# Optimization experiments

Hardware: AMD Instinct MI355X
Metric: run time of the kernel (lower is better)

The kernel has to match this reference:

```python
import jax, jax.numpy as jnp
import numpy as np
from jax import lax

W_MAX = 8
STEP = 1
LEAK = 2
KSIZE = (W_MAX - 1) * (STEP + LEAK)  # 21 = kernel size, padding, and fodep
THETA = 80
FODEP = KSIZE
OUT_CH = 1
NEURONS = 1024


def make_w_kernel_table():
    # StepFireLeak response table: [w_max, ksize], flipped in time
    w_idx = np.arange(W_MAX, dtype=np.float32)[:, None]
    t_idx = np.arange(KSIZE, dtype=np.float32)[None, :]
    w_step = np.maximum(np.floor(1.0 + t_idx / STEP), 0.0)
    w_leak = np.maximum(np.ceil(w_idx + ((w_idx - 1.0) * STEP - t_idx) / LEAK), 0.0)
    table = np.minimum(w_step, w_leak).astype(np.int32)[:, ::-1]
    return jnp.asarray(np.ascontiguousarray(table))


def setup_inputs() -> dict:
    key = jax.random.key(0)
    k1, k2 = jax.random.split(key)
    B, C, S, T = 64, 1, 784, 500
    input_spikes = (jax.random.uniform(k1, (B, C, S, T)) < 0.05).astype(jnp.float32)
    # integer synaptic weights in [0, w_max)
    weight = jax.random.randint(k2, (OUT_CH * NEURONS, C * S), 0, W_MAX, dtype=jnp.int32)
    return {"input_spikes": input_spikes, "weight": weight}


def reference(input_spikes, weight):
    B, C, S, T = input_spikes.shape
    x = input_spikes.reshape(B, C * S, T)
    # expand integer weights into response kernels: [out, in, ksize]
    table = make_w_kernel_table().astype(jnp.float32)
    kern = table[weight]
    pot = lax.conv_general_dilated(
        x, kern, window_strides=(1,), padding=[(KSIZE, KSIZE)],
        dimension_numbers=("NCH", "OIH", "NCH"))
    pot = jnp.rint(pot).astype(jnp.int32)
    Tp = pot.shape[-1]  # T + ksize + 1
    pot = pot.reshape(B, OUT_CH, NEURONS, Tp)
    pot_t = jnp.transpose(pot, (3, 0, 1, 2))  # [Tp, B, C, N]

    def step(dep, p):  # dep: [B, C] int32, p: [B, C, N]
        winner = jnp.argmax(p, axis=-1)  # [B, C]
        val = jnp.take_along_axis(p, winner[..., None], axis=-1)[..., 0]
        cond = ((val > THETA) & (dep == 0)).astype(jnp.int32)  # min_depression == 0
        winners_t = jax.nn.one_hot(winner, NEURONS, dtype=jnp.int32) * cond[..., None]
        new_dep = jnp.maximum(0, dep + cond * (FODEP + 1) - 1)
        return new_dep, winners_t

    dep0 = jnp.zeros((B, OUT_CH), dtype=jnp.int32)
    _, winners = lax.scan(step, dep0, pot_t)  # [Tp, B, C, N]
    return jnp.transpose(winners, (1, 2, 3, 0))  # [B, C, N, Tp]
```

## Files before the change

kernel.cpp:

```cpp
#include <hip/hip_runtime.h>

#define B_DIM 64
#define S_DIM 784
#define T_DIM 500
#define N_DIM 1024
#define TP    522
#define KS    21
#define THETA 80
#define NCHUNK 8
#define CH    66
#define LISTCAP 128

__global__ void k_prep(const int* __restrict__ w, unsigned char* __restrict__ wt9,
                       unsigned* __restrict__ gcnt) {
  unsigned idx = blockIdx.x * 256 + threadIdx.x;
  if (idx < S_DIM * N_DIM) {
    unsigned s = idx >> 10, n = idx & 1023;
    int wv = w[n * S_DIM + s];
    wt9[idx] = wv ? (unsigned char)(9 * (wv - 1)) : (unsigned char)63;
  }
  if (idx < B_DIM * T_DIM) gcnt[idx] = 0;
}

__global__ void k_lists(const float* __restrict__ x, unsigned* __restrict__ gcnt,
                        unsigned short* __restrict__ glist) {
  unsigned idx = blockIdx.x * 256 + threadIdx.x;
  if (idx >= B_DIM * S_DIM * T_DIM) return;
  if (x[idx] != 0.0f) {
    unsigned t = idx % T_DIM;
    unsigned s = (idx / T_DIM) % S_DIM;
    unsigned b = idx / (S_DIM * T_DIM);
    unsigned cell = b * T_DIM + t;
    unsigned pos = atomicAdd(&gcnt[cell], 1u);
    if (pos < LISTCAP) glist[cell * LISTCAP + pos] = (unsigned short)s;
  }
}

__global__ void __launch_bounds__(1024, 8)
k_main(const unsigned char* __restrict__ wt9,
       const unsigned* __restrict__ gcnt,
       const unsigned short* __restrict__ glist,
       unsigned* __restrict__ red) {
  __shared__ unsigned short s_list[87][LISTCAP];
  __shared__ int s_cnt[87];
  __shared__ unsigned smax[CH];

  const int tid = threadIdx.x;
  const int b = blockIdx.y;
  const int lo = blockIdx.x * CH;
  const int hi = min(TP - 1, lo + CH - 1);
  const int t0 = max(0, lo - KS);
  const int n_emit = hi - lo + 1;
  const int nt_in = min(hi, T_DIM - 1) - t0 + 1;

  const unsigned cell0 = (unsigned)b * T_DIM + (unsigned)t0;
  for (int i = tid; i < nt_in; i += 1024)
    s_cnt[i] = min((int)gcnt[cell0 + i], LISTCAP);
  {
    const unsigned* src = (const unsigned*)(glist + (size_t)cell0 * LISTCAP);
    unsigned* dst = (unsigned*)&s_list[0][0];
    const int nw = nt_in * (LISTCAP / 2);
    for (int i = tid; i < nw; i += 1024) dst[i] = src[i];
  }
  for (int i = tid; i < n_emit; i += 1024) smax[i] = 0u;
  __syncthreads();

  int ring[KS + 1];
  #pragma unroll
  for (int i = 0; i <= KS; ++i) ring[i] = 0;

  const unsigned invn = (unsigned)(1023 - tid);

  for (int t = t0; t <= hi; ++t) {
    if (t >= lo) {
      unsigned key = ((unsigned)ring[0] << 10) | invn;
      #pragma unroll
      for (int off = 32; off > 0; off >>= 1) {
        unsigned o = __shfl_xor(key, off, 64);
        key = key > o ? key : o;
      }
      if ((tid & 63) == 0) atomicMax(&smax[t - lo], key);
    }

    if (t < T_DIM) {
      const int li = t - t0;
      const int cnt = __builtin_amdgcn_readfirstlane(s_cnt[li]);
      const unsigned short* lp = &s_list[li][0];
      unsigned long long ca = 0, cb = 0;
      int i = 0;
      for (; i + 1 < cnt; i += 2) {
        unsigned ia = ((unsigned)lp[i] << 10) + tid;
        unsigned ib = ((unsigned)lp[i + 1] << 10) + tid;
        ca += 1ull << wt9[ia];
        cb += 1ull << wt9[ib];
      }
      if (i < cnt) ca += 1ull << wt9[((unsigned)lp[i] << 10) + tid];
      const unsigned long long c = ca + cb;

      const int c1 = (int)(c & 511), c2 = (int)((c >> 9) & 511), c3 = (int)((c >> 18) & 511),
                c4 = (int)((c >> 27) & 511), c5 = (int)((c >> 36) & 511),
                c6 = (int)((c >> 45) & 511), c7 = (int)((c >> 54) & 511);
      const int S7 = c7, S6 = S7 + c6, S5 = S6 + c5, S4 = S5 + c4,
                S3 = S4 + c3, S2 = S3 + c2, S1 = S2 + c1;
      const int O1 = c1, O3 = O1 + c3, O5 = O3 + c5, O7 = O5 + c7;
      const int E2 = c2, E4 = E2 + c4, E6 = E4 + c6;
      const int O31 = O3 - O1, O51 = O5 - O1, O71 = O7 - O1,
                O73 = O7 - O3, O75 = O7 - O5;
      const int E62 = E6 - E2, E64 = E6 - E4;
      int acc = S1;        ring[1]  += acc;
      acc += S2;           ring[2]  += acc;
      acc += S3 - O1;      ring[3]  += acc;
      acc += S4 - E2;      ring[4]  += acc;
      acc += S5 - O31;     ring[5]  += acc;
      acc += S6 - E4;      ring[6]  += acc;
      acc += S7 - O51;     ring[7]  += acc;
      acc -= E62;          ring[8]  += acc;
      acc -= O71;          ring[9]  += acc;
      acc -= E62;          ring[10] += acc;
      acc -= O73;          ring[11] += acc;
      acc -= E62;          ring[12] += acc;
      acc -= O73;          ring[13] += acc;
      acc -= E64;          ring[14] += acc;
      acc -= O73;          ring[15] += acc;
      acc -= E64;          ring[16] += acc;
      acc -= O75;          ring[17] += acc;
      acc -= E64;          ring[18] += acc;
      acc -= O75;          ring[19] += acc;
                           ring[20] += acc;
      acc -= O75;          ring[21] += acc;
    }

    #pragma unroll
    for (int i = 0; i < KS; ++i) ring[i] = ring[i + 1];
    ring[KS] = 0;
  }

  __syncthreads();
  for (int i = tid; i < n_emit; i += 1024)
    red[(unsigned)b * TP + (unsigned)(lo + i)] = smax[i];
}

__global__ void k_scan(const unsigned* __restrict__ red, int* __restrict__ out) {
  int b = threadIdx.x;
  if (b >= B_DIM) return;
  int dep = 0;
  for (int base = 0; base < TP; base += 6) {
    unsigned buf[6];
    #pragma unroll
    for (int k = 0; k < 6; ++k) buf[k] = red[b * TP + base + k];
    #pragma unroll
    for (int k = 0; k < 6; ++k) {
      unsigned key = buf[k];
      int val = (int)(key >> 10);
      bool cond = (val > THETA) && (dep == 0);
      if (cond) {
        int idx = 1023 - (int)(key & 1023);
        out[(b * N_DIM + idx) * TP + base + k] = 1;
        dep = 22;
      }
      dep = max(0, dep - 1);
    }
  }
}

extern "C" void kernel_launch(void* const* d_in, const int* in_sizes, int n_in,
                              void* d_out, int out_size, void* d_ws, size_t ws_size,
                              hipStream_t stream) {
  const float* x = (const float*)d_in[0];
  const int* wgt = (const int*)d_in[1];
  int* out = (int*)d_out;

  unsigned char* wt9    = (unsigned char*)d_ws;
  unsigned* gcnt        = (unsigned*)((char*)d_ws + 802816);
  unsigned short* glist = (unsigned short*)((char*)d_ws + 930816);
  unsigned* red         = (unsigned*)((char*)d_ws + 9122816);

  hipMemsetAsync(d_out, 0, (size_t)out_size * sizeof(int), stream);
  k_prep<<<3136, 256, 0, stream>>>(wgt, wt9, gcnt);
  k_lists<<<(B_DIM * S_DIM * T_DIM + 255) / 256, 256, 0, stream>>>(x, gcnt, glist);
  k_main<<<dim3(NCHUNK, B_DIM), 1024, 0, stream>>>(wt9, gcnt, glist, red);
  k_scan<<<1, 64, 0, stream>>>(red, out);
}
```

Measured before the change: 684.2 us.

## Vectorize spike-list build, pre-shift padded lists, and unroll ring without shifts

The spike-list builder now reads four time steps per thread as a float4 and exits early on all-zero vectors, cutting load count and index arithmetic. In the main kernel, list entries are stored pre-shifted as 32-bit values and padded to a multiple of four with a dummy row of zero-weight entries, so the inner gather reads a uint4 and does four independent table lookups. The register ring buffer is indexed modulo 22 inside a fully unrolled 22-step block, which removes the per-step shift of all ring registers. In exchange, list shared memory doubles, the unrolled body grows, and the launch-bounds occupancy hint is dropped, which may raise register use.

```diff
diff --git a/kernel.cpp b/kernel.cpp
--- a/kernel.cpp
+++ b/kernel.cpp
@@ -10,38 +10,50 @@
 #define NCHUNK 8
 #define CH    66
 #define LISTCAP 128
+#define DUMP_ENTRY (S_DIM << 10)
 
 __global__ void k_prep(const int* __restrict__ w, unsigned char* __restrict__ wt9,
                        unsigned* __restrict__ gcnt) {
   unsigned idx = blockIdx.x * 256 + threadIdx.x;
-  if (idx < S_DIM * N_DIM) {
+  if (idx < (S_DIM + 1) * N_DIM) {
     unsigned s = idx >> 10, n = idx & 1023;
-    int wv = w[n * S_DIM + s];
-    wt9[idx] = wv ? (unsigned char)(9 * (wv - 1)) : (unsigned char)63;
+    unsigned char v = 63;
+    if (s < S_DIM) {
+      int wv = w[n * S_DIM + s];
+      v = wv ? (unsigned char)(9 * (wv - 1)) : (unsigned char)63;
+    }
+    wt9[idx] = v;
   }
   if (idx < B_DIM * T_DIM) gcnt[idx] = 0;
 }
 
-__global__ void k_lists(const float* __restrict__ x, unsigned* __restrict__ gcnt,
+__global__ void k_lists(const float4* __restrict__ x4, unsigned* __restrict__ gcnt,
                         unsigned short* __restrict__ glist) {
   unsigned idx = blockIdx.x * 256 + threadIdx.x;
-  if (idx >= B_DIM * S_DIM * T_DIM) return;
-  if (x[idx] != 0.0f) {
-    unsigned t = idx % T_DIM;
-    unsigned s = (idx / T_DIM) % S_DIM;
-    unsigned b = idx / (S_DIM * T_DIM);
-    unsigned cell = b * T_DIM + t;
-    unsigned pos = atomicAdd(&gcnt[cell], 1u);
-    if (pos < LISTCAP) glist[cell * LISTCAP + pos] = (unsigned short)s;
-  }
-}
-
-__global__ void __launch_bounds__(1024, 8)
+  if (idx >= B_DIM * S_DIM * (T_DIM / 4)) return;
+  float4 v = x4[idx];
+  if (v.x == 0.0f && v.y == 0.0f && v.z == 0.0f && v.w == 0.0f) return;
+  unsigned tq = idx % (T_DIM / 4);
+  unsigned bs = idx / (T_DIM / 4);
+  unsigned s = bs % S_DIM;
+  unsigned b = bs / S_DIM;
+  unsigned cell = b * T_DIM + tq * 4;
+  float f[4] = {v.x, v.y, v.z, v.w};
+  #pragma unroll
+  for (int k = 0; k < 4; ++k) {
+    if (f[k] != 0.0f) {
+      unsigned pos = atomicAdd(&gcnt[cell + k], 1u);
+      if (pos < LISTCAP) glist[(cell + k) * LISTCAP + pos] = (unsigned short)s;
+    }
+  }
+}
+
+__global__ void __launch_bounds__(1024)
 k_main(const unsigned char* __restrict__ wt9,
        const unsigned* __restrict__ gcnt,
        const unsigned short* __restrict__ glist,
        unsigned* __restrict__ red) {
-  __shared__ unsigned short s_list[87][LISTCAP];
+  __shared__ unsigned s_list[87][LISTCAP];
   __shared__ int s_cnt[87];
   __shared__ unsigned smax[CH];
 
@@ -54,85 +66,96 @@
   const int nt_in = min(hi, T_DIM - 1) - t0 + 1;
 
   const unsigned cell0 = (unsigned)b * T_DIM + (unsigned)t0;
-  for (int i = tid; i < nt_in; i += 1024)
-    s_cnt[i] = min((int)gcnt[cell0 + i], LISTCAP);
+  for (int i = tid; i < nt_in; i += 1024) {
+    int c = min((int)gcnt[cell0 + i], LISTCAP);
+    s_cnt[i] = (c + 3) & ~3;
+  }
   {
-    const unsigned* src = (const unsigned*)(glist + (size_t)cell0 * LISTCAP);
-    unsigned* dst = (unsigned*)&s_list[0][0];
-    const int nw = nt_in * (LISTCAP / 2);
-    for (int i = tid; i < nw; i += 1024) dst[i] = src[i];
+    const unsigned short* src = glist + (size_t)cell0 * LISTCAP;
+    const int ne = nt_in * LISTCAP;
+    for (int i = tid; i < ne; i += 1024)
+      s_list[0][i] = (unsigned)src[i] << 10;
   }
   for (int i = tid; i < n_emit; i += 1024) smax[i] = 0u;
   __syncthreads();
-
-  int ring[KS + 1];
+  if (tid < nt_in) {
+    int c = min((int)gcnt[cell0 + tid], LISTCAP);
+    int c4 = (c + 3) & ~3;
+    for (int j = c; j < c4; ++j) s_list[tid][j] = (unsigned)DUMP_ENTRY;
+  }
+  __syncthreads();
+
+  unsigned ring[22];
   #pragma unroll
-  for (int i = 0; i <= KS; ++i) ring[i] = 0;
+  for (int i = 0; i < 22; ++i) ring[i] = 0;
 
   const unsigned invn = (unsigned)(1023 - tid);
 
-  for (int t = t0; t <= hi; ++t) {
-    if (t >= lo) {
-      unsigned key = ((unsigned)ring[0] << 10) | invn;
-      #pragma unroll
-      for (int off = 32; off > 0; off >>= 1) {
-        unsigned o = __shfl_xor(key, off, 64);
-        key = key > o ? key : o;
+  for (int tb = t0; tb <= hi; tb += 22) {
+    #pragma unroll
+    for (int k = 0; k < 22; ++k) {
+      const int t = tb + k;
+      if (t > hi) break;
+
+      if (t >= lo) {
+        unsigned key = (ring[k] << 10) | invn;
+        #pragma unroll
+        for (int off = 32; off > 0; off >>= 1) {
+          unsigned o = __shfl_xor(key, off, 64);
+          key = key > o ? key : o;
+        }
+        if ((tid & 63) == 0) atomicMax(&smax[t - lo], key);
       }
-      if ((tid & 63) == 0) atomicMax(&smax[t - lo], key);
-    }
-
-    if (t < T_DIM) {
-      const int li = t - t0;
-      const int cnt = __builtin_amdgcn_readfirstlane(s_cnt[li]);
-      const unsigned short* lp = &s_list[li][0];
-      unsigned long long ca = 0, cb = 0;
-      int i = 0;
-      for (; i + 1 < cnt; i += 2) {
-        unsigned ia = ((unsigned)lp[i] << 10) + tid;
-        unsigned ib = ((unsigned)lp[i + 1] << 10) + tid;
-        ca += 1ull << wt9[ia];
-        cb += 1ull << wt9[ib];
+      ring[k] = 0;
+
+      if (t < T_DIM) {
+        const int li = t - t0;
+        const int cnt4 = __builtin_amdgcn_readfirstlane(s_cnt[li]);
+        const uint4* lp4 = (const uint4*)&s_list[li][0];
+        unsigned long long c0 = 0, c1 = 0, c2 = 0, c3 = 0;
+        for (int i = 0; i < cnt4; i += 4) {
+          uint4 e = lp4[i >> 2];
+          c0 += 1ull << wt9[e.x + tid];
+          c1 += 1ull << wt9[e.y + tid];
+          c2 += 1ull << wt9[e.z + tid];
+          c3 += 1ull << wt9[e.w + tid];
+        }
+        const unsigned long long c = (c0 + c1) + (c2 + c3);
+
+        const int c1_ = (int)(c & 511), c2_ = (int)((c >> 9) & 511),
+                  c3_ = (int)((c >> 18) & 511), c4_ = (int)((c >> 27) & 511),
+                  c5_ = (int)((c >> 36) & 511), c6_ = (int)((c >> 45) & 511),
+                  c7_ = (int)((c >> 54) & 511);
+        const int S7 = c7_, S6 = S7 + c6_, S5 = S6 + c5_, S4 = S5 + c4_,
+                  S3 = S4 + c3_, S2 = S3 + c2_, S1 = S2 + c1_;
+        const int O1 = c1_, O3 = O1 + c3_, O5 = O3 + c5_, O7 = O5 + c7_;
+        const int E2 = c2_, E4 = E2 + c4_, E6 = E4 + c6_;
+        const int O31 = O3 - O1, O51 = O5 - O1, O71 = O7 - O1,
+                  O73 = O7 - O3, O75 = O7 - O5;
+        const int E62 = E6 - E2, E64 = E6 - E4;
+        int acc = S1;        ring[(k + 1)  % 22] += acc;
+        acc += S2;           ring[(k + 2)  % 22] += acc;
+        acc += S3 - O1;      ring[(k + 3)  % 22] += acc;
+        acc += S4 - E2;      ring[(k + 4)  % 22] += acc;
+        acc += S5 - O31;     ring[(k + 5)  % 22] += acc;
+        acc += S6 - E4;      ring[(k + 6)  % 22] += acc;
+        acc += S7 - O51;     ring[(k + 7)  % 22] += acc;
+        acc -= E62;          ring[(k + 8)  % 22] += acc;
+        acc -= O71;          ring[(k + 9)  % 22] += acc;
+        acc -= E62;          ring[(k + 10) % 22] += acc;
+        acc -= O73;          ring[(k + 11) % 22] += acc;
+        acc -= E62;          ring[(k + 12) % 22] += acc;
+        acc -= O73;          ring[(k + 13) % 22] += acc;
+        acc -= E64;          ring[(k + 14) % 22] += acc;
+        acc -= O73;          ring[(k + 15) % 22] += acc;
+        acc -= E64;          ring[(k + 16) % 22] += acc;
+        acc -= O75;          ring[(k + 17) % 22] += acc;
+        acc -= E64;          ring[(k + 18) % 22] += acc;
+        acc -= O75;          ring[(k + 19) % 22] += acc;
+                             ring[(k + 20) % 22] += acc;
+        acc -= O75;          ring[(k + 21) % 22] += acc;
       }
-      if (i < cnt) ca += 1ull << wt9[((unsigned)lp[i] << 10) + tid];
-      const unsigned long long c = ca + cb;
-
-      const int c1 = (int)(c & 511), c2 = (int)((c >> 9) & 511), c3 = (int)((c >> 18) & 511),
-                c4 = (int)((c >> 27) & 511), c5 = (int)((c >> 36) & 511),
-                c6 = (int)((c >> 45) & 511), c7 = (int)((c >> 54) & 511);
-      const int S7 = c7, S6 = S7 + c6, S5 = S6 + c5, S4 = S5 + c4,
-                S3 = S4 + c3, S2 = S3 + c2, S1 = S2 + c1;
-      const int O1 = c1, O3 = O1 + c3, O5 = O3 + c5, O7 = O5 + c7;
-      const int E2 = c2, E4 = E2 + c4, E6 = E4 + c6;
-      const int O31 = O3 - O1, O51 = O5 - O1, O71 = O7 - O1,
-                O73 = O7 - O3, O75 = O7 - O5;
-      const int E62 = E6 - E2, E64 = E6 - E4;
-      int acc = S1;        ring[1]  += acc;
-      acc += S2;           ring[2]  += acc;
-      acc += S3 - O1;      ring[3]  += acc;
-      acc += S4 - E2;      ring[4]  += acc;
-      acc += S5 - O31;     ring[5]  += acc;
-      acc += S6 - E4;      ring[6]  += acc;
-      acc += S7 - O51;     ring[7]  += acc;
-      acc -= E62;          ring[8]  += acc;
-      acc -= O71;          ring[9]  += acc;
-      acc -= E62;          ring[10] += acc;
-      acc -= O73;          ring[11] += acc;
-      acc -= E62;          ring[12] += acc;
-      acc -= O73;          ring[13] += acc;
-      acc -= E64;          ring[14] += acc;
-      acc -= O73;          ring[15] += acc;
-      acc -= E64;          ring[16] += acc;
-      acc -= O75;          ring[17] += acc;
-      acc -= E64;          ring[18] += acc;
-      acc -= O75;          ring[19] += acc;
-                           ring[20] += acc;
-      acc -= O75;          ring[21] += acc;
-    }
-
-    #pragma unroll
-    for (int i = 0; i < KS; ++i) ring[i] = ring[i + 1];
-    ring[KS] = 0;
+    }
   }
 
   __syncthreads();
@@ -171,13 +194,14 @@
   int* out = (int*)d_out;
 
   unsigned char* wt9    = (unsigned char*)d_ws;
-  unsigned* gcnt        = (unsigned*)((char*)d_ws + 802816);
-  unsigned short* glist = (unsigned short*)((char*)d_ws + 930816);
-  unsigned* red         = (unsigned*)((char*)d_ws + 9122816);
+  unsigned* gcnt        = (unsigned*)((char*)d_ws + 803840);
+  unsigned short* glist = (unsigned short*)((char*)d_ws + 931840);
+  unsigned* red         = (unsigned*)((char*)d_ws + 9123840);
 
   hipMemsetAsync(d_out, 0, (size_t)out_size * sizeof(int), stream);
-  k_prep<<<3136, 256, 0, stream>>>(wgt, wt9, gcnt);
-  k_lists<<<(B_DIM * S_DIM * T_DIM + 255) / 256, 256, 0, stream>>>(x, gcnt, glist);
+  k_prep<<<((S_DIM + 1) * N_DIM + 255) / 256, 256, 0, stream>>>(wgt, wt9, gcnt);
+  k_lists<<<(B_DIM * S_DIM * (T_DIM / 4) + 255) / 256, 256, 0, stream>>>(
+      (const float4*)x, gcnt, glist);
   k_main<<<dim3(NCHUNK, B_DIM), 1024, 0, stream>>>(wt9, gcnt, glist, red);
   k_scan<<<1, 64, 0, stream>>>(red, out);
 }
```

After: 689.3 us. Within noise of the previous version (+0.7%).

## Vectorize spike list build, fuse output zeroing, pad lists for 8-wide gathers

Applied to the files above, without the earlier changes.

The spike-list kernel now reads the input as float4 and also zeroes the output with int4 stores, which replaces the separate memset. A dummy weight row (index S_DIM, value 63) is appended so that each per-time spike list can be padded to a multiple of 8 entries. The main loop then reads 8 list entries with one uint4 shared load and issues 8 gathers spread over 4 accumulators. Padding adds extra gathers from the dummy row and an extra barrier, in exchange for fewer LDS loads, a branch-free inner loop and one fewer launch.

```diff
diff --git a/kernel.cpp b/kernel.cpp
--- a/kernel.cpp
+++ b/kernel.cpp
@@ -10,30 +10,46 @@
 #define NCHUNK 8
 #define CH    66
 #define LISTCAP 128
+#define NSPIKE_THREADS (B_DIM * S_DIM * (T_DIM / 4))
+#define NFILL4 ((B_DIM * N_DIM * TP) / 4)
 
 __global__ void k_prep(const int* __restrict__ w, unsigned char* __restrict__ wt9,
                        unsigned* __restrict__ gcnt) {
   unsigned idx = blockIdx.x * 256 + threadIdx.x;
-  if (idx < S_DIM * N_DIM) {
+  if (idx < (S_DIM + 1) * N_DIM) {
     unsigned s = idx >> 10, n = idx & 1023;
-    int wv = w[n * S_DIM + s];
-    wt9[idx] = wv ? (unsigned char)(9 * (wv - 1)) : (unsigned char)63;
+    unsigned char v = 63;
+    if (s < S_DIM) {
+      int wv = w[n * S_DIM + s];
+      v = wv ? (unsigned char)(9 * (wv - 1)) : (unsigned char)63;
+    }
+    wt9[idx] = v;
   }
   if (idx < B_DIM * T_DIM) gcnt[idx] = 0;
 }
 
-__global__ void k_lists(const float* __restrict__ x, unsigned* __restrict__ gcnt,
-                        unsigned short* __restrict__ glist) {
+__global__ void k_listsfill(const float4* __restrict__ x4, unsigned* __restrict__ gcnt,
+                            unsigned short* __restrict__ glist, int4* __restrict__ out4) {
   unsigned idx = blockIdx.x * 256 + threadIdx.x;
-  if (idx >= B_DIM * S_DIM * T_DIM) return;
-  if (x[idx] != 0.0f) {
-    unsigned t = idx % T_DIM;
-    unsigned s = (idx / T_DIM) % S_DIM;
-    unsigned b = idx / (S_DIM * T_DIM);
-    unsigned cell = b * T_DIM + t;
-    unsigned pos = atomicAdd(&gcnt[cell], 1u);
-    if (pos < LISTCAP) glist[cell * LISTCAP + pos] = (unsigned short)s;
-  }
+  if (idx < NSPIKE_THREADS) {
+    float4 v = x4[idx];
+    if (!(v.x == 0.0f && v.y == 0.0f && v.z == 0.0f && v.w == 0.0f)) {
+      unsigned tq = idx % (T_DIM / 4);
+      unsigned bs = idx / (T_DIM / 4);
+      unsigned s = bs % S_DIM;
+      unsigned b = bs / S_DIM;
+      unsigned cell = b * T_DIM + tq * 4;
+      float f[4] = {v.x, v.y, v.z, v.w};
+      #pragma unroll
+      for (int k = 0; k < 4; ++k) {
+        if (f[k] != 0.0f) {
+          unsigned pos = atomicAdd(&gcnt[cell + k], 1u);
+          if (pos < LISTCAP) glist[(cell + k) * LISTCAP + pos] = (unsigned short)s;
+        }
+      }
+    }
+  }
+  if (idx < NFILL4) out4[idx] = make_int4(0, 0, 0, 0);
 }
 
 __global__ void __launch_bounds__(1024, 8)
@@ -54,8 +70,10 @@
   const int nt_in = min(hi, T_DIM - 1) - t0 + 1;
 
   const unsigned cell0 = (unsigned)b * T_DIM + (unsigned)t0;
-  for (int i = tid; i < nt_in; i += 1024)
-    s_cnt[i] = min((int)gcnt[cell0 + i], LISTCAP);
+  for (int i = tid; i < nt_in; i += 1024) {
+    int c = min((int)gcnt[cell0 + i], LISTCAP);
+    s_cnt[i] = (c + 7) & ~7;
+  }
   {
     const unsigned* src = (const unsigned*)(glist + (size_t)cell0 * LISTCAP);
     unsigned* dst = (unsigned*)&s_list[0][0];
@@ -63,6 +81,12 @@
     for (int i = tid; i < nw; i += 1024) dst[i] = src[i];
   }
   for (int i = tid; i < n_emit; i += 1024) smax[i] = 0u;
+  __syncthreads();
+  if (tid < nt_in) {
+    int c = min((int)gcnt[cell0 + tid], LISTCAP);
+    int c8 = (c + 7) & ~7;
+    for (int j = c; j < c8; ++j) s_list[tid][j] = (unsigned short)S_DIM;
+  }
   __syncthreads();
 
   int ring[KS + 1];
@@ -84,26 +108,38 @@
 
     if (t < T_DIM) {
       const int li = t - t0;
-      const int cnt = __builtin_amdgcn_readfirstlane(s_cnt[li]);
-      const unsigned short* lp = &s_list[li][0];
-      unsigned long long ca = 0, cb = 0;
-      int i = 0;
-      for (; i + 1 < cnt; i += 2) {
-        unsigned ia = ((unsigned)lp[i] << 10) + tid;
-        unsigned ib = ((unsigned)lp[i + 1] << 10) + tid;
-        ca += 1ull << wt9[ia];
-        cb += 1ull << wt9[ib];
-      }
-      if (i < cnt) ca += 1ull << wt9[((unsigned)lp[i] << 10) + tid];
-      const unsigned long long c = ca + cb;
-
-      const int c1 = (int)(c & 511), c2 = (int)((c >> 9) & 511), c3 = (int)((c >> 18) & 511),
-                c4 = (int)((c >> 27) & 511), c5 = (int)((c >> 36) & 511),
-                c6 = (int)((c >> 45) & 511), c7 = (int)((c >> 54) & 511);
-      const int S7 = c7, S6 = S7 + c6, S5 = S6 + c5, S4 = S5 + c4,
-                S3 = S4 + c3, S2 = S3 + c2, S1 = S2 + c1;
-      const int O1 = c1, O3 = O1 + c3, O5 = O3 + c5, O7 = O5 + c7;
-      const int E2 = c2, E4 = E2 + c4, E6 = E4 + c6;
+      const int cnt8 = __builtin_amdgcn_readfirstlane(s_cnt[li]);
+      const uint4* lp4 = (const uint4*)&s_list[li][0];
+      unsigned long long c0 = 0, c1 = 0, c2 = 0, c3 = 0;
+      for (int i = 0; i < cnt8; i += 8) {
+        uint4 e = lp4[i >> 3];
+        unsigned a0 = ((e.x << 10) & 0x000FFC00u) + tid;
+        unsigned a1 = ((e.x >> 6)  & 0x000FFC00u) + tid;
+        unsigned a2 = ((e.y << 10) & 0x000FFC00u) + tid;
+        unsigned a3 = ((e.y >> 6)  & 0x000FFC00u) + tid;
+        unsigned a4 = ((e.z << 10) & 0x000FFC00u) + tid;
+        unsigned a5 = ((e.z >> 6)  & 0x000FFC00u) + tid;
+        unsigned a6 = ((e.w << 10) & 0x000FFC00u) + tid;
+        unsigned a7 = ((e.w >> 6)  & 0x000FFC00u) + tid;
+        c0 += 1ull << wt9[a0];
+        c1 += 1ull << wt9[a1];
+        c2 += 1ull << wt9[a2];
+        c3 += 1ull << wt9[a3];
+        c0 += 1ull << wt9[a4];
+        c1 += 1ull << wt9[a5];
+        c2 += 1ull << wt9[a6];
+        c3 += 1ull << wt9[a7];
+      }
+      const unsigned long long c = (c0 + c1) + (c2 + c3);
+
+      const int c1_ = (int)(c & 511), c2_ = (int)((c >> 9) & 511),
+                c3_ = (int)((c >> 18) & 511), c4_ = (int)((c >> 27) & 511),
+                c5_ = (int)((c >> 36) & 511), c6_ = (int)((c >> 45) & 511),
+                c7_ = (int)((c >> 54) & 511);
+      const int S7 = c7_, S6 = S7 + c6_, S5 = S6 + c5_, S4 = S5 + c4_,
+                S3 = S4 + c3_, S2 = S3 + c2_, S1 = S2 + c1_;
+      const int O1 = c1_, O3 = O1 + c3_, O5 = O3 + c5_, O7 = O5 + c7_;
+      const int E2 = c2_, E4 = E2 + c4_, E6 = E4 + c6_;
       const int O31 = O3 - O1, O51 = O5 - O1, O71 = O7 - O1,
                 O73 = O7 - O3, O75 = O7 - O5;
       const int E62 = E6 - E2, E64 = E6 - E4;
@@ -171,13 +207,13 @@
   int* out = (int*)d_out;
 
   unsigned char* wt9    = (unsigned char*)d_ws;
-  unsigned* gcnt        = (unsigned*)((char*)d_ws + 802816);
-  unsigned short* glist = (unsigned short*)((char*)d_ws + 930816);
-  unsigned* red         = (unsigned*)((char*)d_ws + 9122816);
-
-  hipMemsetAsync(d_out, 0, (size_t)out_size * sizeof(int), stream);
-  k_prep<<<3136, 256, 0, stream>>>(wgt, wt9, gcnt);
-  k_lists<<<(B_DIM * S_DIM * T_DIM + 255) / 256, 256, 0, stream>>>(x, gcnt, glist);
+  unsigned* gcnt        = (unsigned*)((char*)d_ws + 803840);
+  unsigned short* glist = (unsigned short*)((char*)d_ws + 931840);
+  unsigned* red         = (unsigned*)((char*)d_ws + 9123840);
+
+  k_prep<<<((S_DIM + 1) * N_DIM + 255) / 256, 256, 0, stream>>>(wgt, wt9, gcnt);
+  k_listsfill<<<(NFILL4 + 255) / 256, 256, 0, stream>>>(
+      (const float4*)x, gcnt, glist, (int4*)out);
   k_main<<<dim3(NCHUNK, B_DIM), 1024, 0, stream>>>(wt9, gcnt, glist, red);
   k_scan<<<1, 64, 0, stream>>>(red, out);
 }
```

Measured after the change: 756.0 us. 10.5% more time.
